# Kernel optimization log

Measured on AMD Instinct MI355X. Metric: run time of the kernel, lower is better.

## Reference

```python
import jax, jax.numpy as jnp
import numpy as np

N_NODES = 10000
N_EDGES = 200000
F = 128
NB = 20
LN_EPS = 1e-5

act = jax.nn.silu

def mlp2(x, W1, b1, W2, b2):
    # two-layer MLP: Linear -> silu -> Linear (weights stored [in, out])
    h = act(jnp.dot(x, W1) + b1)
    return jnp.dot(h, W2) + b2

def mlp2_nobias(x, W1, W2):
    return jnp.dot(act(jnp.dot(x, W1)), W2)

def layernorm(x, g, b):
    mu = jnp.mean(x, axis=-1, keepdims=True)
    var = jnp.mean(jnp.square(x - mu), axis=-1, keepdims=True)
    return (x - mu) * jax.lax.rsqrt(var + LN_EPS) * g + b

def setup_inputs() -> dict:
    key = jax.random.key(0)
    ks = jax.random.split(key, 32)
    s = 1.0 / np.sqrt(F)
    d = {
        "atom_node": jax.random.normal(ks[0], (N_NODES, F), jnp.float32),
        "force_node": jax.random.normal(ks[1], (N_NODES, 3, F), jnp.float32),
        "disp_node": jax.random.normal(ks[2], (N_NODES, 3, F), jnp.float32),
        "disp_edge": jax.random.normal(ks[3], (N_EDGES, 3), jnp.float32),
        "dist_edge": jax.random.uniform(ks[4], (N_EDGES, NB), jnp.float32),
        "edge_index": jax.random.randint(ks[5], (2, N_EDGES), 0, N_NODES, jnp.int32),
        # inv_message_nodepart
        "nmp_W1": jax.random.normal(ks[6], (F, F), jnp.float32) * s,
        "nmp_b1": jnp.zeros((F,), jnp.float32),
        "nmp_W2": jax.random.normal(ks[7], (F, F), jnp.float32) * s,
        "nmp_b2": jnp.zeros((F,), jnp.float32),
        # inv_message_edgepart
        "emp_W": jax.random.normal(ks[8], (NB, F), jnp.float32) * (1.0 / np.sqrt(NB)),
        "emp_b": jnp.zeros((F,), jnp.float32),
        # equiv_message1
        "eq1_W1": jax.random.normal(ks[9], (F, F), jnp.float32) * s,
        "eq1_b1": jnp.zeros((F,), jnp.float32),
        "eq1_W2": jax.random.normal(ks[10], (F, F), jnp.float32) * s,
        "eq1_b2": jnp.zeros((F,), jnp.float32),
        # equiv_message2
        "eq2_W1": jax.random.normal(ks[11], (F, F), jnp.float32) * s,
        "eq2_b1": jnp.zeros((F,), jnp.float32),
        "eq2_W2": jax.random.normal(ks[12], (F, F), jnp.float32) * s,
        "eq2_b2": jnp.zeros((F,), jnp.float32),
        # equiv_message3 (no bias)
        "eq3_W1": jax.random.normal(ks[13], (F, F), jnp.float32) * s,
        "eq3_W2": jax.random.normal(ks[14], (F, F), jnp.float32) * s,
        # inv_update
        "upd_W1": jax.random.normal(ks[15], (F, F), jnp.float32) * s,
        "upd_b1": jnp.zeros((F,), jnp.float32),
        "upd_W2": jax.random.normal(ks[16], (F, F), jnp.float32) * s,
        "upd_b2": jnp.zeros((F,), jnp.float32),
        # LayerNorm
        "ln_g": jnp.ones((F,), jnp.float32),
        "ln_b": jnp.zeros((F,), jnp.float32),
    }
    return d

def reference(atom_node, force_node, disp_node, disp_edge, dist_edge, edge_index,
              nmp_W1, nmp_b1, nmp_W2, nmp_b2, emp_W, emp_b,
              eq1_W1, eq1_b1, eq1_W2, eq1_b2,
              eq2_W1, eq2_b1, eq2_W2, eq2_b2,
              eq3_W1, eq3_W2,
              upd_W1, upd_b1, upd_W2, upd_b2,
              ln_g, ln_b):
    n = atom_node.shape[0]
    src = edge_index[0]
    dst = edge_index[1]
    seg = lambda x: jax.ops.segment_sum(x, src, num_segments=n)

    # invariant message: edge part * node parts gathered at both endpoints
    h = mlp2(atom_node, nmp_W1, nmp_b1, nmp_W2, nmp_b2)            # [N, F]
    e = jnp.dot(dist_edge, emp_W) + emp_b                           # [E, F]
    inv_message = e * h[src] * h[dst]                               # [E, F]
    atom_node = atom_node + seg(inv_message)

    # equivariant message 1: radial MLP * displacement vectors
    eq1 = mlp2(inv_message, eq1_W1, eq1_b1, eq1_W2, eq1_b2)[:, None, :] \
          * disp_edge[:, :, None]                                   # [E, 3, F]
    agg1 = seg(eq1)                                                 # [N, 3, F]
    force_node = force_node + agg1

    # equivariant message 2: edge MLP * neighbor displacement features (pre-update)
    eq2 = mlp2(inv_message, eq2_W1, eq2_b1, eq2_W2, eq2_b2)[:, None, :] \
          * disp_node[dst]                                          # [E, 3, F]
    disp_node = disp_node + seg(eq2)

    # equivariant message 3: scatter-then-gather of agg1 with invariant gate
    eq3_inv = mlp2_nobias(atom_node, eq3_W1, eq3_W2)                # [N, F]
    eq3 = eq3_inv[dst][:, None, :] * agg1[dst]                      # [E, 3, F]
    disp_node = disp_node + seg(eq3)

    # invariant update coupling force and displacement channels
    inv_update = mlp2(atom_node, upd_W1, upd_b1, upd_W2, upd_b2) \
                 * jnp.sum(-force_node * disp_node, axis=-2)        # [N, F]
    atom_node = layernorm(atom_node + inv_update, ln_g, ln_b)
    return (atom_node, force_node, disp_node)
```

## Files before the change

kernel.cpp:

```cpp
#include <hip/hip_runtime.h>
#include <hip/hip_bf16.h>

#define F 128
#define NB 20
#define KP 32
#define HSTRIDE 136
#define HROWS_STRIDE 140

typedef __attribute__((ext_vector_type(8))) short short8;
typedef __attribute__((ext_vector_type(4))) short short4v;
typedef __attribute__((ext_vector_type(4))) float floatx4;

__device__ __forceinline__ float silu_f(float x) {
    return x * __builtin_amdgcn_rcpf(1.0f + __expf(-x));
}
__device__ __forceinline__ float bfs2f(short s) {
    unsigned int u = ((unsigned int)(unsigned short)s) << 16;
    float f; __builtin_memcpy(&f, &u, 4); return f;
}
__device__ __forceinline__ float lo_bf(unsigned int u) { return bfs2f((short)(u & 0xFFFF)); }
__device__ __forceinline__ float hi_bf(unsigned int u) { return bfs2f((short)(u >> 16)); }
__device__ __forceinline__ unsigned int pack_bf2(float d, float v) {
    __hip_bfloat16 db = __float2bfloat16(d), vb = __float2bfloat16(v);
    return (unsigned int)*(unsigned short*)&db
         | ((unsigned int)*(unsigned short*)&vb << 16);
}

__device__ __forceinline__ void stage_issue(const __hip_bfloat16* W, int t,
                                            short8 wreg[4]) {
#pragma unroll
    for (int r = 0; r < 4; ++r)
        wreg[r] = *(const short8*)(W + (size_t)(r * 512 + t) * 8);
}
__device__ __forceinline__ void stage_write(__hip_bfloat16* wbuf, int t,
                                            const short8 wreg[4]) {
#pragma unroll
    for (int r = 0; r < 4; ++r) {
        const int c = r * 512 + t;
        *(short8*)(wbuf + (size_t)(c >> 4) * HSTRIDE + (c & 15) * 8) = wreg[r];
    }
}

template<typename OUT_T, bool BIAS>
__global__ __launch_bounds__(256) void fused_mlp_kernel(
    const __hip_bfloat16* __restrict__ X,
    const __hip_bfloat16* __restrict__ Wt1, const float* __restrict__ b1,
    const __hip_bfloat16* __restrict__ Wt2, const float* __restrict__ b2,
    OUT_T* __restrict__ Y, int Mp)
{
    __shared__ __hip_bfloat16 hid[128 * HSTRIDE];
    const int t = threadIdx.x;
    const int wave = t >> 6;
    const int lane = t & 63;
    const int quad = lane >> 4;
    const int l16  = lane & 15;
    const int eloc0 = wave * 32;
    const int e0 = blockIdx.x * 128 + eloc0;

    floatx4 acc[8][2];
#pragma unroll
    for (int ft = 0; ft < 8; ++ft)
#pragma unroll
        for (int et = 0; et < 2; ++et)
            acc[ft][et] = (floatx4){0.f, 0.f, 0.f, 0.f};

#pragma unroll
    for (int ks = 0; ks < 4; ++ks) {
        const int k0 = ks * 32 + quad * 8;
        short8 bx[2], aw[8];
#pragma unroll
        for (int et = 0; et < 2; ++et)
            bx[et] = *(const short8*)(X + (size_t)(e0 + et * 16 + l16) * F + k0);
#pragma unroll
        for (int ft = 0; ft < 8; ++ft)
            aw[ft] = *(const short8*)(Wt1 + (size_t)(ft * 16 + l16) * F + k0);
#pragma unroll
        for (int ft = 0; ft < 8; ++ft)
#pragma unroll
            for (int et = 0; et < 2; ++et)
                acc[ft][et] = __builtin_amdgcn_mfma_f32_16x16x32_bf16(
                    aw[ft], bx[et], acc[ft][et], 0, 0, 0);
    }

#pragma unroll
    for (int ft = 0; ft < 8; ++ft) {
        const int feat = ft * 16 + quad * 4;
        floatx4 bv = (floatx4){0.f, 0.f, 0.f, 0.f};
        if (BIAS) bv = *(const floatx4*)(b1 + feat);
#pragma unroll
        for (int et = 0; et < 2; ++et) {
            const int el = eloc0 + et * 16 + l16;
            __align__(8) __hip_bfloat16 tmp[4];
#pragma unroll
            for (int r = 0; r < 4; ++r)
                tmp[r] = __float2bfloat16(silu_f(acc[ft][et][r] + bv[r]));
            *(short4v*)(hid + (size_t)el * HSTRIDE + feat) = *(const short4v*)tmp;
        }
    }
    __builtin_amdgcn_sched_barrier(0);

#pragma unroll
    for (int ft = 0; ft < 8; ++ft)
#pragma unroll
        for (int et = 0; et < 2; ++et)
            acc[ft][et] = (floatx4){0.f, 0.f, 0.f, 0.f};

#pragma unroll
    for (int ks = 0; ks < 4; ++ks) {
        const int k0 = ks * 32 + quad * 8;
        short8 bx[2], aw[8];
#pragma unroll
        for (int et = 0; et < 2; ++et)
            bx[et] = *(const short8*)(hid + (size_t)(eloc0 + et * 16 + l16) * HSTRIDE + k0);
#pragma unroll
        for (int ft = 0; ft < 8; ++ft)
            aw[ft] = *(const short8*)(Wt2 + (size_t)(ft * 16 + l16) * F + k0);
#pragma unroll
        for (int ft = 0; ft < 8; ++ft)
#pragma unroll
            for (int et = 0; et < 2; ++et)
                acc[ft][et] = __builtin_amdgcn_mfma_f32_16x16x32_bf16(
                    aw[ft], bx[et], acc[ft][et], 0, 0, 0);
    }

#pragma unroll
    for (int ft = 0; ft < 8; ++ft) {
        const int feat = ft * 16 + quad * 4;
        floatx4 bv = (floatx4){0.f, 0.f, 0.f, 0.f};
        if (BIAS) bv = *(const floatx4*)(b2 + feat);
#pragma unroll
        for (int et = 0; et < 2; ++et) {
            const int e = e0 + et * 16 + l16;
            if (sizeof(OUT_T) == 2) {
                __align__(8) __hip_bfloat16 tmp[4];
#pragma unroll
                for (int r = 0; r < 4; ++r)
                    tmp[r] = __float2bfloat16(acc[ft][et][r] + bv[r]);
                *(short4v*)((__hip_bfloat16*)Y + (size_t)e * F + feat) = *(const short4v*)tmp;
            } else {
                floatx4 v;
#pragma unroll
                for (int r = 0; r < 4; ++r) v[r] = acc[ft][et][r] + bv[r];
                *(floatx4*)((float*)Y + (size_t)e * F + feat) = v;
            }
        }
    }
}

template<typename OUTA, typename OUTB, bool BIASA, bool BIASB>
__global__ __launch_bounds__(512, 4) void dual_mlp_kernel(
    const __hip_bfloat16* X,
    const __hip_bfloat16* __restrict__ W1a, const float* __restrict__ b1a,
    const __hip_bfloat16* __restrict__ W2a, const float* __restrict__ b2a,
    const __hip_bfloat16* __restrict__ W1b, const float* __restrict__ b1b,
    const __hip_bfloat16* __restrict__ W2b, const float* __restrict__ b2b,
    OUTA* __restrict__ Q1, OUTB* Q2, int Mp)
{
    __shared__ __hip_bfloat16 hid[128 * HSTRIDE];
    __shared__ __hip_bfloat16 wbuf[128 * HSTRIDE];
    const int t = threadIdx.x;
    const int wave = t >> 6;
    const int rg   = wave >> 1;
    const int wf   = wave & 1;
    const int lane = t & 63;
    const int quad = lane >> 4;
    const int l16  = lane & 15;
    const int eloc0 = rg * 32;
    const int e0 = blockIdx.x * 128 + eloc0;
    const int fbase = wf * 64;

    short8 bxk[4][2];
#pragma unroll
    for (int ks = 0; ks < 4; ++ks)
#pragma unroll
        for (int et = 0; et < 2; ++et)
            bxk[ks][et] = *(const short8*)(X + (size_t)(e0 + et * 16 + l16) * F
                                           + ks * 32 + quad * 8);

    short8 wreg[4];
    floatx4 acc[4][2];

    stage_issue(W1a, t, wreg);
    stage_write(wbuf, t, wreg);
    __syncthreads();

    stage_issue(W2a, t, wreg);
    __builtin_amdgcn_sched_barrier(0);
#pragma unroll
    for (int ft = 0; ft < 4; ++ft)
#pragma unroll
        for (int et = 0; et < 2; ++et)
            acc[ft][et] = (floatx4){0.f, 0.f, 0.f, 0.f};
#pragma unroll
    for (int ks = 0; ks < 4; ++ks) {
        const int k0 = ks * 32 + quad * 8;
        short8 aw[4];
#pragma unroll
        for (int ft = 0; ft < 4; ++ft)
            aw[ft] = *(const short8*)(wbuf + (size_t)(fbase + ft * 16 + l16) * HSTRIDE + k0);
#pragma unroll
        for (int ft = 0; ft < 4; ++ft)
#pragma unroll
            for (int et = 0; et < 2; ++et)
                acc[ft][et] = __builtin_amdgcn_mfma_f32_16x16x32_bf16(
                    aw[ft], bxk[ks][et], acc[ft][et], 0, 0, 0);
    }
#pragma unroll
    for (int ft = 0; ft < 4; ++ft) {
        const int feat = fbase + ft * 16 + quad * 4;
        floatx4 bv = (floatx4){0.f, 0.f, 0.f, 0.f};
        if (BIASA) bv = *(const floatx4*)(b1a + feat);
#pragma unroll
        for (int et = 0; et < 2; ++et) {
            const int el = eloc0 + et * 16 + l16;
            __align__(8) __hip_bfloat16 tmp[4];
#pragma unroll
            for (int r = 0; r < 4; ++r)
                tmp[r] = __float2bfloat16(silu_f(acc[ft][et][r] + bv[r]));
            *(short4v*)(hid + (size_t)el * HSTRIDE + feat) = *(const short4v*)tmp;
        }
    }
    __syncthreads();
    stage_write(wbuf, t, wreg);
    __syncthreads();

    stage_issue(W1b, t, wreg);
    __builtin_amdgcn_sched_barrier(0);
#pragma unroll
    for (int ft = 0; ft < 4; ++ft)
#pragma unroll
        for (int et = 0; et < 2; ++et)
            acc[ft][et] = (floatx4){0.f, 0.f, 0.f, 0.f};
#pragma unroll
    for (int ks = 0; ks < 4; ++ks) {
        const int k0 = ks * 32 + quad * 8;
        short8 bh[2], aw[4];
#pragma unroll
        for (int et = 0; et < 2; ++et)
            bh[et] = *(const short8*)(hid + (size_t)(eloc0 + et * 16 + l16) * HSTRIDE + k0);
#pragma unroll
        for (int ft = 0; ft < 4; ++ft)
            aw[ft] = *(const short8*)(wbuf + (size_t)(fbase + ft * 16 + l16) * HSTRIDE + k0);
#pragma unroll
        for (int ft = 0; ft < 4; ++ft)
#pragma unroll
            for (int et = 0; et < 2; ++et)
                acc[ft][et] = __builtin_amdgcn_mfma_f32_16x16x32_bf16(
                    aw[ft], bh[et], acc[ft][et], 0, 0, 0);
    }
#pragma unroll
    for (int ft = 0; ft < 4; ++ft) {
        const int feat = fbase + ft * 16 + quad * 4;
        floatx4 bv = (floatx4){0.f, 0.f, 0.f, 0.f};
        if (BIASA) bv = *(const floatx4*)(b2a + feat);
#pragma unroll
        for (int et = 0; et < 2; ++et) {
            const int e = e0 + et * 16 + l16;
            if (sizeof(OUTA) == 2) {
                __align__(8) __hip_bfloat16 tmp[4];
#pragma unroll
                for (int r = 0; r < 4; ++r)
                    tmp[r] = __float2bfloat16(acc[ft][et][r] + bv[r]);
                *(short4v*)((__hip_bfloat16*)Q1 + (size_t)e * F + feat) = *(const short4v*)tmp;
            } else {
                floatx4 v;
#pragma unroll
                for (int r = 0; r < 4; ++r) v[r] = acc[ft][et][r] + bv[r];
                *(floatx4*)((float*)Q1 + (size_t)e * F + feat) = v;
            }
        }
    }
    __syncthreads();
    stage_write(wbuf, t, wreg);
    __syncthreads();

    stage_issue(W2b, t, wreg);
    __builtin_amdgcn_sched_barrier(0);
#pragma unroll
    for (int ft = 0; ft < 4; ++ft)
#pragma unroll
        for (int et = 0; et < 2; ++et)
            acc[ft][et] = (floatx4){0.f, 0.f, 0.f, 0.f};
#pragma unroll
    for (int ks = 0; ks < 4; ++ks) {
        const int k0 = ks * 32 + quad * 8;
        short8 aw[4];
#pragma unroll
        for (int ft = 0; ft < 4; ++ft)
            aw[ft] = *(const short8*)(wbuf + (size_t)(fbase + ft * 16 + l16) * HSTRIDE + k0);
#pragma unroll
        for (int ft = 0; ft < 4; ++ft)
#pragma unroll
            for (int et = 0; et < 2; ++et)
                acc[ft][et] = __builtin_amdgcn_mfma_f32_16x16x32_bf16(
                    aw[ft], bxk[ks][et], acc[ft][et], 0, 0, 0);
    }
#pragma unroll
    for (int ft = 0; ft < 4; ++ft) {
        const int feat = fbase + ft * 16 + quad * 4;
        floatx4 bv = (floatx4){0.f, 0.f, 0.f, 0.f};
        if (BIASB) bv = *(const floatx4*)(b1b + feat);
#pragma unroll
        for (int et = 0; et < 2; ++et) {
            const int el = eloc0 + et * 16 + l16;
            __align__(8) __hip_bfloat16 tmp[4];
#pragma unroll
            for (int r = 0; r < 4; ++r)
                tmp[r] = __float2bfloat16(silu_f(acc[ft][et][r] + bv[r]));
            *(short4v*)(hid + (size_t)el * HSTRIDE + feat) = *(const short4v*)tmp;
        }
    }
    __syncthreads();
    stage_write(wbuf, t, wreg);
    __syncthreads();

#pragma unroll
    for (int ft = 0; ft < 4; ++ft)
#pragma unroll
        for (int et = 0; et < 2; ++et)
            acc[ft][et] = (floatx4){0.f, 0.f, 0.f, 0.f};
#pragma unroll
    for (int ks = 0; ks < 4; ++ks) {
        const int k0 = ks * 32 + quad * 8;
        short8 bh[2], aw[4];
#pragma unroll
        for (int et = 0; et < 2; ++et)
            bh[et] = *(const short8*)(hid + (size_t)(eloc0 + et * 16 + l16) * HSTRIDE + k0);
#pragma unroll
        for (int ft = 0; ft < 4; ++ft)
            aw[ft] = *(const short8*)(wbuf + (size_t)(fbase + ft * 16 + l16) * HSTRIDE + k0);
#pragma unroll
        for (int ft = 0; ft < 4; ++ft)
#pragma unroll
            for (int et = 0; et < 2; ++et)
                acc[ft][et] = __builtin_amdgcn_mfma_f32_16x16x32_bf16(
                    aw[ft], bh[et], acc[ft][et], 0, 0, 0);
    }
#pragma unroll
    for (int ft = 0; ft < 4; ++ft) {
        const int feat = fbase + ft * 16 + quad * 4;
        floatx4 bv = (floatx4){0.f, 0.f, 0.f, 0.f};
        if (BIASB) bv = *(const floatx4*)(b2b + feat);
#pragma unroll
        for (int et = 0; et < 2; ++et) {
            const int e = e0 + et * 16 + l16;
            if (sizeof(OUTB) == 2) {
                __align__(8) __hip_bfloat16 tmp[4];
#pragma unroll
                for (int r = 0; r < 4; ++r)
                    tmp[r] = __float2bfloat16(acc[ft][et][r] + bv[r]);
                *(short4v*)((__hip_bfloat16*)Q2 + (size_t)e * F + feat) = *(const short4v*)tmp;
            } else {
                floatx4 v;
#pragma unroll
                for (int r = 0; r < 4; ++r) v[r] = acc[ft][et][r] + bv[r];
                *(floatx4*)((float*)Q2 + (size_t)e * F + feat) = v;
            }
        }
    }
}

__global__ __launch_bounds__(256) void edge_inv_mfma_kernel(
    const __hip_bfloat16* __restrict__ dist_p,
    const __hip_bfloat16* __restrict__ empWt,
    const float* __restrict__ emp_b, const __hip_bfloat16* __restrict__ h,
    const int* __restrict__ src_p, const int* __restrict__ dst_p,
    __hip_bfloat16* __restrict__ Xbf, int E)
{
    __shared__ __hip_bfloat16 hrows[256 * HROWS_STRIDE];
    __shared__ int ridx[256];
    const int t = threadIdx.x;
    const int wave = t >> 6;
    const int lane = t & 63;
    const int quad = lane >> 4;
    const int l16  = lane & 15;
    const int e0b = blockIdx.x * 128;
    const int e0 = e0b + wave * 32;

    {
        const int le = (t < 128) ? t : (t - 128);
        const int e = e0b + le;
        const int idx = (e < E) ? ((t < 128) ? src_p[e] : dst_p[e]) : 0;
        ridx[t] = idx;
    }
    __syncthreads();

#pragma unroll
    for (int i = 0; i < 16; ++i) {
        const int idx = i * 256 + t;
        const int r = idx >> 4, part = idx & 15;
        const short8 v = *(const short8*)(h + (size_t)ridx[r] * F + part * 8);
        const short4v lo = __builtin_shufflevector(v, v, 0, 1, 2, 3);
        const short4v hi = __builtin_shufflevector(v, v, 4, 5, 6, 7);
        *(short4v*)(hrows + (size_t)r * HROWS_STRIDE + part * 8)     = lo;
        *(short4v*)(hrows + (size_t)r * HROWS_STRIDE + part * 8 + 4) = hi;
    }

    short8 bx[2], aw[8];
#pragma unroll
    for (int et = 0; et < 2; ++et)
        bx[et] = *(const short8*)(dist_p + (size_t)(e0 + et * 16 + l16) * KP + quad * 8);
#pragma unroll
    for (int ft = 0; ft < 8; ++ft)
        aw[ft] = *(const short8*)(empWt + (size_t)(ft * 16 + l16) * KP + quad * 8);

    floatx4 acc[8][2];
#pragma unroll
    for (int ft = 0; ft < 8; ++ft)
#pragma unroll
        for (int et = 0; et < 2; ++et)
            acc[ft][et] = __builtin_amdgcn_mfma_f32_16x16x32_bf16(
                aw[ft], bx[et], (floatx4){0.f, 0.f, 0.f, 0.f}, 0, 0, 0);

    __syncthreads();

    int eidx[2];
#pragma unroll
    for (int et = 0; et < 2; ++et) eidx[et] = e0 + et * 16 + l16;

#pragma unroll
    for (int ft = 0; ft < 8; ++ft) {
        const int feat = ft * 16 + quad * 4;
        const floatx4 bv = *(const floatx4*)(emp_b + feat);
#pragma unroll
        for (int et = 0; et < 2; ++et) {
            const int le = wave * 32 + et * 16 + l16;
            const short4v hs = *(const short4v*)(hrows + (size_t)le * HROWS_STRIDE + feat);
            const short4v hd = *(const short4v*)(hrows + (size_t)(128 + le) * HROWS_STRIDE + feat);
            const bool v = eidx[et] < E;
            __align__(8) __hip_bfloat16 tmp[4];
#pragma unroll
            for (int r = 0; r < 4; ++r) {
                const float m = v ? (acc[ft][et][r] + bv[r]) * bfs2f(hs[r]) * bfs2f(hd[r])
                                  : 0.0f;
                tmp[r] = __float2bfloat16(m);
            }
            *(short4v*)(Xbf + (size_t)eidx[et] * F + feat) = *(const short4v*)tmp;
        }
    }
}


__global__ void prep_weights_kernel(
    const float* __restrict__ W0, const float* __restrict__ W1,
    const float* __restrict__ W2, const float* __restrict__ W3,
    const float* __restrict__ W4, const float* __restrict__ W5,
    const float* __restrict__ W6, const float* __restrict__ W7,
    const float* __restrict__ W8, const float* __restrict__ W9,
    __hip_bfloat16* __restrict__ Wt)
{
    const int t = blockIdx.x * 256 + threadIdx.x;
    if (t >= 10 * F * F) return;
    const int w = t >> 14;
    const int idx = t & (F * F - 1);
    const int n = idx >> 7;
    const int k = idx & 127;
    const float* W = (w == 0) ? W0 : (w == 1) ? W1 : (w == 2) ? W2 : (w == 3) ? W3
                   : (w == 4) ? W4 : (w == 5) ? W5 : (w == 6) ? W6 : (w == 7) ? W7
                   : (w == 8) ? W8 : W9;
    Wt[t] = __float2bfloat16(W[k * F + n]);
}

__global__ void prep_empw_kernel(const float* __restrict__ emp_W,
                                 __hip_bfloat16* __restrict__ empWt)
{
    const int t = blockIdx.x * 256 + threadIdx.x;
    if (t >= F * KP) return;
    const int n = t >> 5;
    const int k = t & (KP - 1);
    empWt[t] = __float2bfloat16(k < NB ? emp_W[k * F + n] : 0.0f);
}

__global__ void cast_pad_kernel(const float* __restrict__ src,
                                __hip_bfloat16* __restrict__ dst,
                                int n_valid, int n_total)
{
    const int stride = gridDim.x * blockDim.x;
    for (int i = blockIdx.x * blockDim.x + threadIdx.x; i < n_total; i += stride)
        dst[i] = __float2bfloat16(i < n_valid ? src[i] : 0.0f);
}

__global__ void pad_zero_bf_kernel(__hip_bfloat16* __restrict__ dst,
                                   int from, int to)
{
    const int i = from + blockIdx.x * 256 + threadIdx.x;
    if (i < to) dst[i] = __float2bfloat16(0.0f);
}


__global__ void zero_counts_kernel(int* __restrict__ counts, int N) {
    const int stride = gridDim.x * blockDim.x;
    for (int i = blockIdx.x * blockDim.x + threadIdx.x; i < N; i += stride)
        counts[i] = 0;
}

__global__ void csr_count_kernel(const int* __restrict__ src,
                                 int* __restrict__ counts, int E) {
    const int stride = gridDim.x * blockDim.x;
    for (int e = blockIdx.x * blockDim.x + threadIdx.x; e < E; e += stride)
        atomicAdd(&counts[src[e]], 1);
}

__global__ __launch_bounds__(1024) void csr_scan_kernel(
    const int* __restrict__ counts, int* __restrict__ offsets,
    int* __restrict__ cursor, int N)
{
    constexpr int T = 1024;
    const int t = threadIdx.x;
    const int per = (N + T - 1) / T;
    const int base = t * per;
    int lsum = 0;
    for (int i = 0; i < per; ++i) {
        int idx = base + i;
        if (idx < N) lsum += counts[idx];
    }
    __shared__ int s[T];
    s[t] = lsum;
    __syncthreads();
    for (int off = 1; off < T; off <<= 1) {
        int v = (t >= off) ? s[t - off] : 0;
        __syncthreads();
        s[t] += v;
        __syncthreads();
    }
    int run = s[t] - lsum;
    for (int i = 0; i < per; ++i) {
        int idx = base + i;
        if (idx < N) {
            offsets[idx] = run;
            cursor[idx] = run;
            run += counts[idx];
        }
    }
    if (t == T - 1) offsets[N] = run;
}

__global__ void csr_perm_kernel(const int* __restrict__ src,
                                const int* __restrict__ dst,
                                const float* __restrict__ disp_edge,
                                const float* __restrict__ dist_edge,
                                int* __restrict__ cursor,
                                int* __restrict__ src_p,
                                int* __restrict__ dst_p,
                                float* __restrict__ de_p,
                                __hip_bfloat16* __restrict__ dist_p, int E) {
    const int stride = gridDim.x * blockDim.x;
    for (int e = blockIdx.x * blockDim.x + threadIdx.x; e < E; e += stride) {
        const int s = src[e];
        const int pos = atomicAdd(&cursor[s], 1);
        src_p[pos] = s;
        dst_p[pos] = dst[e];
        de_p[3 * pos + 0] = disp_edge[3 * e + 0];
        de_p[3 * pos + 1] = disp_edge[3 * e + 1];
        de_p[3 * pos + 2] = disp_edge[3 * e + 2];
        __align__(16) __hip_bfloat16 tmp[KP];
#pragma unroll
        for (int k = 0; k < KP; ++k)
            tmp[k] = __float2bfloat16(k < NB ? dist_edge[(size_t)e * NB + k] : 0.0f);
#pragma unroll
        for (int q = 0; q < 4; ++q)
            *(short8*)(dist_p + (size_t)pos * KP + q * 8) = ((const short8*)tmp)[q];
    }
}


__global__ __launch_bounds__(256) void gather_inv_kernel(
    const __hip_bfloat16* __restrict__ inv_msg, const int* __restrict__ offsets,
    const float* __restrict__ atom,
    float* __restrict__ atom_new, __hip_bfloat16* __restrict__ atom_new_bf, int N)
{
    const int n = blockIdx.x * 4 + (threadIdx.x >> 6);
    if (n >= N) return;
    const int f0 = (threadIdx.x & 63) * 2;
    const int p0 = offsets[n], p1 = offsets[n + 1];
    float a0 = 0.0f, a1 = 0.0f;
    for (int p = p0; p < p1; ++p) {
        const unsigned int u = *(const unsigned int*)(inv_msg + (size_t)p * F + f0);
        a0 += lo_bf(u);
        a1 += hi_bf(u);
    }
    const float2 av = *(const float2*)(atom + (size_t)n * F + f0);
    const float v0 = av.x + a0, v1 = av.y + a1;
    *(float2*)(atom_new + (size_t)n * F + f0) = make_float2(v0, v1);
    __hip_bfloat16 b0 = __float2bfloat16(v0), b1 = __float2bfloat16(v1);
    *(ushort2*)(atom_new_bf + (size_t)n * F + f0) =
        make_ushort2(*(unsigned short*)&b0, *(unsigned short*)&b1);
}

__global__ __launch_bounds__(256) void gather_eq1_kernel(
    const __hip_bfloat16* __restrict__ eqm, const float* __restrict__ de_p,
    const int* __restrict__ offsets,
    const float* __restrict__ force, const float* __restrict__ disp_node,
    const __hip_bfloat16* __restrict__ eq3i_bf,
    float* __restrict__ out_force, ushort2* __restrict__ pk, int N)
{
    const int n = blockIdx.x * 4 + (threadIdx.x >> 6);
    if (n >= N) return;
    const int f0 = (threadIdx.x & 63) * 2;
    const int p0 = offsets[n], p1 = offsets[n + 1];
    float a00 = 0.f, a01 = 0.f, a10 = 0.f, a11 = 0.f, a20 = 0.f, a21 = 0.f;
    for (int p = p0; p < p1; ++p) {
        const unsigned int u = *(const unsigned int*)(eqm + (size_t)p * F + f0);
        const float m0 = lo_bf(u), m1 = hi_bf(u);
        const float d0 = de_p[(size_t)p * 3 + 0];
        const float d1 = de_p[(size_t)p * 3 + 1];
        const float d2 = de_p[(size_t)p * 3 + 2];
        a00 = fmaf(m0, d0, a00); a01 = fmaf(m1, d0, a01);
        a10 = fmaf(m0, d1, a10); a11 = fmaf(m1, d1, a11);
        a20 = fmaf(m0, d2, a20); a21 = fmaf(m1, d2, a21);
    }
    const unsigned int ug = *(const unsigned int*)(eq3i_bf + (size_t)n * F + f0);
    const float g0 = lo_bf(ug), g1 = hi_bf(ug);
    const size_t b = (size_t)n * 3 * F + f0;

    float2 f;
    f = *(const float2*)(force + b);
    *(float2*)(out_force + b) = make_float2(f.x + a00, f.y + a01);
    f = *(const float2*)(force + b + F);
    *(float2*)(out_force + b + F) = make_float2(f.x + a10, f.y + a11);
    f = *(const float2*)(force + b + 2 * F);
    *(float2*)(out_force + b + 2 * F) = make_float2(f.x + a20, f.y + a21);

    float2 dn;
    dn = *(const float2*)(disp_node + b);
    *(uint2*)(pk + b) = make_uint2(pack_bf2(dn.x, g0 * a00), pack_bf2(dn.y, g1 * a01));
    dn = *(const float2*)(disp_node + b + F);
    *(uint2*)(pk + b + F) = make_uint2(pack_bf2(dn.x, g0 * a10), pack_bf2(dn.y, g1 * a11));
    dn = *(const float2*)(disp_node + b + 2 * F);
    *(uint2*)(pk + b + 2 * F) = make_uint2(pack_bf2(dn.x, g0 * a20), pack_bf2(dn.y, g1 * a21));
}

__global__ __launch_bounds__(256) void gather_eq23_kernel(
    const __hip_bfloat16* __restrict__ eqm2, const ushort2* __restrict__ pk,
    const float* __restrict__ disp_node,
    const int* __restrict__ dst_p, const int* __restrict__ offsets,
    float* __restrict__ out_disp, int N)
{
    const int n = blockIdx.x * 4 + (threadIdx.x >> 6);
    if (n >= N) return;
    const int f0 = (threadIdx.x & 63) * 2;
    const int p0 = offsets[n], p1 = offsets[n + 1];
    float a00 = 0.f, a01 = 0.f, a10 = 0.f, a11 = 0.f, a20 = 0.f, a21 = 0.f;
    int d = (p0 < p1) ? dst_p[p0] : 0;
    for (int p = p0; p < p1; ++p) {
        const int dn = (p + 1 < p1) ? dst_p[p + 1] : 0;
        const unsigned int u = *(const unsigned int*)(eqm2 + (size_t)p * F + f0);
        const float m0 = lo_bf(u), m1 = hi_bf(u);
        const size_t pb = (size_t)d * 3 * F + f0;
        const uint2 c0 = *(const uint2*)(pk + pb);
        const uint2 c1 = *(const uint2*)(pk + pb + F);
        const uint2 c2 = *(const uint2*)(pk + pb + 2 * F);
        a00 += m0 * lo_bf(c0.x) + hi_bf(c0.x);
        a01 += m1 * lo_bf(c0.y) + hi_bf(c0.y);
        a10 += m0 * lo_bf(c1.x) + hi_bf(c1.x);
        a11 += m1 * lo_bf(c1.y) + hi_bf(c1.y);
        a20 += m0 * lo_bf(c2.x) + hi_bf(c2.x);
        a21 += m1 * lo_bf(c2.y) + hi_bf(c2.y);
        d = dn;
    }
    const size_t b = (size_t)n * 3 * F + f0;
    float2 dn2;
    dn2 = *(const float2*)(disp_node + b);
    *(float2*)(out_disp + b) = make_float2(dn2.x + a00, dn2.y + a01);
    dn2 = *(const float2*)(disp_node + b + F);
    *(float2*)(out_disp + b + F) = make_float2(dn2.x + a10, dn2.y + a11);
    dn2 = *(const float2*)(disp_node + b + 2 * F);
    *(float2*)(out_disp + b + 2 * F) = make_float2(dn2.x + a20, dn2.y + a21);
}


__global__ __launch_bounds__(256) void update_ln_kernel(
    const float* __restrict__ atom_new, const float* __restrict__ upd,
    const float* __restrict__ out_force, const float* __restrict__ out_disp,
    const float* __restrict__ ln_g, const float* __restrict__ ln_b,
    float* __restrict__ out_atom, int N)
{
    const int n = blockIdx.x * 4 + (threadIdx.x >> 6);
    if (n >= N) return;
    const int f0 = (threadIdx.x & 63) * 2;
    const size_t b = (size_t)n * 3 * F + f0;

    const float2 fo0 = *(const float2*)(out_force + b);
    const float2 fo1 = *(const float2*)(out_force + b + F);
    const float2 fo2 = *(const float2*)(out_force + b + 2 * F);
    const float2 dl0 = *(const float2*)(out_disp + b);
    const float2 dl1 = *(const float2*)(out_disp + b + F);
    const float2 dl2 = *(const float2*)(out_disp + b + 2 * F);
    const float s0 = -(fo0.x * dl0.x + fo1.x * dl1.x + fo2.x * dl2.x);
    const float s1 = -(fo0.y * dl0.y + fo1.y * dl1.y + fo2.y * dl2.y);

    const float2 an = *(const float2*)(atom_new + (size_t)n * F + f0);
    const float2 up = *(const float2*)(upd + (size_t)n * F + f0);
    const float y0 = an.x + up.x * s0;
    const float y1 = an.y + up.y * s1;

    float sy = y0 + y1, syy = y0 * y0 + y1 * y1;
#pragma unroll
    for (int m = 1; m < 64; m <<= 1) {
        sy  += __shfl_xor(sy, m);
        syy += __shfl_xor(syy, m);
    }
    const float mu = sy * (1.0f / F);
    float var = syy * (1.0f / F) - mu * mu;
    if (var < 0.0f) var = 0.0f;
    const float rstd = rsqrtf(var + 1e-5f);

    const float2 gg = *(const float2*)(ln_g + f0);
    const float2 bb = *(const float2*)(ln_b + f0);
    *(float2*)(out_atom + (size_t)n * F + f0) =
        make_float2((y0 - mu) * rstd * gg.x + bb.x,
                    (y1 - mu) * rstd * gg.y + bb.y);
}

extern "C" void kernel_launch(void* const* d_in, const int* in_sizes, int n_in,
                              void* d_out, int out_size, void* d_ws, size_t ws_size,
                              hipStream_t stream)
{
    const float* atom_node  = (const float*)d_in[0];
    const float* force_node = (const float*)d_in[1];
    const float* disp_node  = (const float*)d_in[2];
    const float* disp_edge  = (const float*)d_in[3];
    const float* dist_edge  = (const float*)d_in[4];
    const int*   edge_index = (const int*)d_in[5];
    const float* nmp_W1 = (const float*)d_in[6];
    const float* nmp_b1 = (const float*)d_in[7];
    const float* nmp_W2 = (const float*)d_in[8];
    const float* nmp_b2 = (const float*)d_in[9];
    const float* emp_W  = (const float*)d_in[10];
    const float* emp_b  = (const float*)d_in[11];
    const float* eq1_W1 = (const float*)d_in[12];
    const float* eq1_b1 = (const float*)d_in[13];
    const float* eq1_W2 = (const float*)d_in[14];
    const float* eq1_b2 = (const float*)d_in[15];
    const float* eq2_W1 = (const float*)d_in[16];
    const float* eq2_b1 = (const float*)d_in[17];
    const float* eq2_W2 = (const float*)d_in[18];
    const float* eq2_b2 = (const float*)d_in[19];
    const float* eq3_W1 = (const float*)d_in[20];
    const float* eq3_W2 = (const float*)d_in[21];
    const float* upd_W1 = (const float*)d_in[22];
    const float* upd_b1 = (const float*)d_in[23];
    const float* upd_W2 = (const float*)d_in[24];
    const float* upd_b2 = (const float*)d_in[25];
    const float* ln_g   = (const float*)d_in[26];
    const float* ln_b   = (const float*)d_in[27];

    const int N = in_sizes[0] / F;
    const int E = in_sizes[4] / NB;
    const int Mp  = ((E + 127) / 128) * 128;
    const int Mp2 = ((N + 127) / 128) * 128;
    const int* src = edge_index;
    const int* dst = edge_index + E;
    const int nF = N * F, n3F = N * 3 * F;

    float* out_atom  = (float*)d_out;
    float* out_force = out_atom + (size_t)nF;
    float* out_disp  = out_force + (size_t)n3F;

    char* p = (char*)d_ws;
    int* counts  = (int*)p;
    int* offsets = counts + N;
    int* cursor  = offsets + (N + 1);
    int* src_p   = cursor + N;
    int* dst_p   = src_p + E;
    size_t off = (size_t)(3 * N + 1 + 2 * E) * sizeof(int);
    off = (off + 63) & ~(size_t)63;
    float* de_p = (float*)(p + off); off += (size_t)3 * E * sizeof(float);
    off = (off + 63) & ~(size_t)63;
    __hip_bfloat16* dist_p = (__hip_bfloat16*)(p + off); off += (size_t)Mp * KP * 2;
    __hip_bfloat16* empWt  = (__hip_bfloat16*)(p + off); off += (size_t)F * KP * 2;

    __hip_bfloat16* h_bf        = (__hip_bfloat16*)(p + off); off += (size_t)Mp2 * F * 2;
    __hip_bfloat16* atom_bf     = (__hip_bfloat16*)(p + off); off += (size_t)Mp2 * F * 2;
    __hip_bfloat16* atom_new_bf = (__hip_bfloat16*)(p + off); off += (size_t)Mp2 * F * 2;
    __hip_bfloat16* eq3i_bf     = (__hip_bfloat16*)(p + off); off += (size_t)Mp2 * F * 2;
    off = (off + 63) & ~(size_t)63;
    float* atom_new = (float*)(p + off); off += (size_t)nF * 4;
    float* upd_f    = (float*)(p + off); off += (size_t)Mp2 * F * 4;
    ushort2* pk     = (ushort2*)(p + off); off += (size_t)n3F * sizeof(ushort2);
    off = (off + 63) & ~(size_t)63;
    __hip_bfloat16* Xbf = (__hip_bfloat16*)(p + off); off += (size_t)Mp * F * 2;
    __hip_bfloat16* Q1  = (__hip_bfloat16*)(p + off); off += (size_t)Mp * F * 2;
    __hip_bfloat16* Q2  = Xbf;
    __hip_bfloat16* Wt  = (__hip_bfloat16*)(p + off);
    __hip_bfloat16* Wt_eq1a = Wt + 0 * F * F;
    __hip_bfloat16* Wt_eq1b = Wt + 1 * F * F;
    __hip_bfloat16* Wt_eq2a = Wt + 2 * F * F;
    __hip_bfloat16* Wt_eq2b = Wt + 3 * F * F;
    __hip_bfloat16* Wt_nmpa = Wt + 4 * F * F;
    __hip_bfloat16* Wt_nmpb = Wt + 5 * F * F;
    __hip_bfloat16* Wt_eq3a = Wt + 6 * F * F;
    __hip_bfloat16* Wt_eq3b = Wt + 7 * F * F;
    __hip_bfloat16* Wt_upda = Wt + 8 * F * F;
    __hip_bfloat16* Wt_updb = Wt + 9 * F * F;

    prep_weights_kernel<<<(10 * F * F + 255) / 256, 256, 0, stream>>>(
        eq1_W1, eq1_W2, eq2_W1, eq2_W2, nmp_W1, nmp_W2, eq3_W1, eq3_W2,
        upd_W1, upd_W2, Wt);
    prep_empw_kernel<<<(F * KP + 255) / 256, 256, 0, stream>>>(emp_W, empWt);
    cast_pad_kernel<<<512, 256, 0, stream>>>(atom_node, atom_bf, nF, Mp2 * F);
    pad_zero_bf_kernel<<<(Mp2 * F - nF + 255) / 256, 256, 0, stream>>>(
        atom_new_bf, nF, Mp2 * F);
    zero_counts_kernel<<<64, 256, 0, stream>>>(counts, N);
    csr_count_kernel<<<256, 256, 0, stream>>>(src, counts, E);
    csr_scan_kernel<<<1, 1024, 0, stream>>>(counts, offsets, cursor, N);
    csr_perm_kernel<<<256, 256, 0, stream>>>(src, dst, disp_edge, dist_edge,
                                             cursor, src_p, dst_p, de_p, dist_p, E);

    fused_mlp_kernel<__hip_bfloat16, true><<<Mp2 / 128, 256, 0, stream>>>(
        atom_bf, Wt_nmpa, nmp_b1, Wt_nmpb, nmp_b2, h_bf, Mp2);

    edge_inv_mfma_kernel<<<Mp / 128, 256, 0, stream>>>(
        dist_p, empWt, emp_b, h_bf, src_p, dst_p, Xbf, E);
    gather_inv_kernel<<<(N + 3) / 4, 256, 0, stream>>>(Xbf, offsets, atom_node,
                                                       atom_new, atom_new_bf, N);

    dual_mlp_kernel<__hip_bfloat16, float, false, true><<<Mp2 / 128, 512, 0, stream>>>(
        atom_new_bf, Wt_eq3a, nullptr, Wt_eq3b, nullptr,
        Wt_upda, upd_b1, Wt_updb, upd_b2, eq3i_bf, upd_f, Mp2);

    dual_mlp_kernel<__hip_bfloat16, __hip_bfloat16, true, true>
        <<<Mp / 128, 512, 0, stream>>>(
        Xbf, Wt_eq1a, eq1_b1, Wt_eq1b, eq1_b2,
        Wt_eq2a, eq2_b1, Wt_eq2b, eq2_b2, Q1, Q2, Mp);

    gather_eq1_kernel<<<(N + 3) / 4, 256, 0, stream>>>(
        Q1, de_p, offsets, force_node, disp_node, eq3i_bf, out_force, pk, N);
    gather_eq23_kernel<<<(N + 3) / 4, 256, 0, stream>>>(
        Q2, pk, disp_node, dst_p, offsets, out_disp, N);

    update_ln_kernel<<<(N + 3) / 4, 256, 0, stream>>>(
        atom_new, upd_f, out_force, out_disp, ln_g, ln_b, out_atom, N);
}
```

Measured before the change: 442.4 us.

## Merge node and edge dual-MLP launches, fragment-swizzle weight LDS, fuse LN into gather

Merges the two dual-MLP launches (node-side eq3/update and edge-side eq1/eq2) into one grid, choosing pointers at runtime by block index. Weight staging in LDS moves to a per-MFMA-fragment layout with an XOR swizzle, which removes the padded stride and is meant to cut LDS bank conflicts and shrink LDS use. The update+layernorm kernel is folded into the eq2/eq3 gather kernel, so out_disp is used from registers rather than reread. Runtime bias checks and selection branches add a little per-block overhead.

Result: faster. 424.7 us (-4.0%).

```diff
diff --git a/kernel.cpp b/kernel.cpp
--- a/kernel.cpp
+++ b/kernel.cpp
@@ -32,12 +32,16 @@
     for (int r = 0; r < 4; ++r)
         wreg[r] = *(const short8*)(W + (size_t)(r * 512 + t) * 8);
 }
-__device__ __forceinline__ void stage_write(__hip_bfloat16* wbuf, int t,
-                                            const short8 wreg[4]) {
+__device__ __forceinline__ void stage_write_frag(__hip_bfloat16* wbuf, int t,
+                                                 const short8 wreg[4]) {
 #pragma unroll
     for (int r = 0; r < 4; ++r) {
-        const int c = r * 512 + t;
-        *(short8*)(wbuf + (size_t)(c >> 4) * HSTRIDE + (c & 15) * 8) = wreg[r];
+        const int c0 = r * 512 + t;
+        const int n = c0 >> 4, p = c0 & 15;
+        const int ks = p >> 2;
+        const int frag = ((n >> 6) * 4 + ((n >> 4) & 3)) * 4 + ks;
+        const int lam = (((p & 3) * 16) + (n & 15)) ^ (ks << 1);
+        *(short8*)(wbuf + (size_t)frag * 512 + lam * 8) = wreg[r];
     }
 }
 
@@ -147,17 +151,34 @@
     }
 }
 
-template<typename OUTA, typename OUTB, bool BIASA, bool BIASB>
-__global__ __launch_bounds__(512, 4) void dual_mlp_kernel(
-    const __hip_bfloat16* X,
-    const __hip_bfloat16* __restrict__ W1a, const float* __restrict__ b1a,
-    const __hip_bfloat16* __restrict__ W2a, const float* __restrict__ b2a,
-    const __hip_bfloat16* __restrict__ W1b, const float* __restrict__ b1b,
-    const __hip_bfloat16* __restrict__ W2b, const float* __restrict__ b2b,
-    OUTA* __restrict__ Q1, OUTB* Q2, int Mp)
+__global__ __launch_bounds__(512, 4) void dual_mlp2_kernel(
+    const __hip_bfloat16* Xe,
+    const __hip_bfloat16* __restrict__ W1a_e, const float* __restrict__ b1a_e,
+    const __hip_bfloat16* __restrict__ W2a_e, const float* __restrict__ b2a_e,
+    const __hip_bfloat16* __restrict__ W1b_e, const float* __restrict__ b1b_e,
+    const __hip_bfloat16* __restrict__ W2b_e, const float* __restrict__ b2b_e,
+    __hip_bfloat16* __restrict__ Q1e, __hip_bfloat16* Q2e, int ntile_e,
+    const __hip_bfloat16* __restrict__ Xn,
+    const __hip_bfloat16* __restrict__ W1a_n,
+    const __hip_bfloat16* __restrict__ W2a_n,
+    const __hip_bfloat16* __restrict__ W1b_n, const float* __restrict__ b1b_n,
+    const __hip_bfloat16* __restrict__ W2b_n, const float* __restrict__ b2b_n,
+    __hip_bfloat16* __restrict__ Q1n, float* __restrict__ Q2n)
 {
     __shared__ __hip_bfloat16 hid[128 * HSTRIDE];
-    __shared__ __hip_bfloat16 wbuf[128 * HSTRIDE];
+    __shared__ __hip_bfloat16 wbuf[32 * 512];
+    const bool nn = (int)blockIdx.x >= ntile_e;
+    const int tile = nn ? ((int)blockIdx.x - ntile_e) : (int)blockIdx.x;
+    const __hip_bfloat16* X   = nn ? Xn : Xe;
+    const __hip_bfloat16* W1a = nn ? W1a_n : W1a_e;
+    const __hip_bfloat16* W2a = nn ? W2a_n : W2a_e;
+    const __hip_bfloat16* W1b = nn ? W1b_n : W1b_e;
+    const __hip_bfloat16* W2b = nn ? W2b_n : W2b_e;
+    const float* b1a = nn ? nullptr : b1a_e;
+    const float* b2a = nn ? nullptr : b2a_e;
+    const float* b1b = nn ? b1b_n : b1b_e;
+    const float* b2b = nn ? b2b_n : b2b_e;
+
     const int t = threadIdx.x;
     const int wave = t >> 6;
     const int rg   = wave >> 1;
@@ -166,7 +187,7 @@
     const int quad = lane >> 4;
     const int l16  = lane & 15;
     const int eloc0 = rg * 32;
-    const int e0 = blockIdx.x * 128 + eloc0;
+    const int e0 = tile * 128 + eloc0;
     const int fbase = wf * 64;
 
     short8 bxk[4][2];
@@ -181,7 +202,7 @@
     floatx4 acc[4][2];
 
     stage_issue(W1a, t, wreg);
-    stage_write(wbuf, t, wreg);
+    stage_write_frag(wbuf, t, wreg);
     __syncthreads();
 
     stage_issue(W2a, t, wreg);
@@ -193,11 +214,11 @@
             acc[ft][et] = (floatx4){0.f, 0.f, 0.f, 0.f};
 #pragma unroll
     for (int ks = 0; ks < 4; ++ks) {
-        const int k0 = ks * 32 + quad * 8;
         short8 aw[4];
 #pragma unroll
         for (int ft = 0; ft < 4; ++ft)
-            aw[ft] = *(const short8*)(wbuf + (size_t)(fbase + ft * 16 + l16) * HSTRIDE + k0);
+            aw[ft] = *(const short8*)(wbuf + ((wf * 4 + ft) * 4 + ks) * 512
+                                      + ((lane ^ (ks << 1)) * 8));
 #pragma unroll
         for (int ft = 0; ft < 4; ++ft)
 #pragma unroll
@@ -209,7 +230,7 @@
     for (int ft = 0; ft < 4; ++ft) {
         const int feat = fbase + ft * 16 + quad * 4;
         floatx4 bv = (floatx4){0.f, 0.f, 0.f, 0.f};
-        if (BIASA) bv = *(const floatx4*)(b1a + feat);
+        if (b1a) bv = *(const floatx4*)(b1a + feat);
 #pragma unroll
         for (int et = 0; et < 2; ++et) {
             const int el = eloc0 + et * 16 + l16;
@@ -221,7 +242,7 @@
         }
     }
     __syncthreads();
-    stage_write(wbuf, t, wreg);
+    stage_write_frag(wbuf, t, wreg);
     __syncthreads();
 
     stage_issue(W1b, t, wreg);
@@ -240,7 +261,8 @@
             bh[et] = *(const short8*)(hid + (size_t)(eloc0 + et * 16 + l16) * HSTRIDE + k0);
 #pragma unroll
         for (int ft = 0; ft < 4; ++ft)
-            aw[ft] = *(const short8*)(wbuf + (size_t)(fbase + ft * 16 + l16) * HSTRIDE + k0);
+            aw[ft] = *(const short8*)(wbuf + ((wf * 4 + ft) * 4 + ks) * 512
+                                      + ((lane ^ (ks << 1)) * 8));
 #pragma unroll
         for (int ft = 0; ft < 4; ++ft)
 #pragma unroll
@@ -252,26 +274,19 @@
     for (int ft = 0; ft < 4; ++ft) {
         const int feat = fbase + ft * 16 + quad * 4;
         floatx4 bv = (floatx4){0.f, 0.f, 0.f, 0.f};
-        if (BIASA) bv = *(const floatx4*)(b2a + feat);
+        if (b2a) bv = *(const floatx4*)(b2a + feat);
 #pragma unroll
         for (int et = 0; et < 2; ++et) {
             const int e = e0 + et * 16 + l16;
-            if (sizeof(OUTA) == 2) {
-                __align__(8) __hip_bfloat16 tmp[4];
-#pragma unroll
-                for (int r = 0; r < 4; ++r)
-                    tmp[r] = __float2bfloat16(acc[ft][et][r] + bv[r]);
-                *(short4v*)((__hip_bfloat16*)Q1 + (size_t)e * F + feat) = *(const short4v*)tmp;
-            } else {
-                floatx4 v;
-#pragma unroll
-                for (int r = 0; r < 4; ++r) v[r] = acc[ft][et][r] + bv[r];
-                *(floatx4*)((float*)Q1 + (size_t)e * F + feat) = v;
-            }
+            __align__(8) __hip_bfloat16 tmp[4];
+#pragma unroll
+            for (int r = 0; r < 4; ++r)
+                tmp[r] = __float2bfloat16(acc[ft][et][r] + bv[r]);
+            *(short4v*)((nn ? Q1n : Q1e) + (size_t)e * F + feat) = *(const short4v*)tmp;
         }
     }
     __syncthreads();
-    stage_write(wbuf, t, wreg);
+    stage_write_frag(wbuf, t, wreg);
     __syncthreads();
 
     stage_issue(W2b, t, wreg);
@@ -283,11 +298,11 @@
             acc[ft][et] = (floatx4){0.f, 0.f, 0.f, 0.f};
 #pragma unroll
     for (int ks = 0; ks < 4; ++ks) {
-        const int k0 = ks * 32 + quad * 8;
         short8 aw[4];
 #pragma unroll
         for (int ft = 0; ft < 4; ++ft)
-            aw[ft] = *(const short8*)(wbuf + (size_t)(fbase + ft * 16 + l16) * HSTRIDE + k0);
+            aw[ft] = *(const short8*)(wbuf + ((wf * 4 + ft) * 4 + ks) * 512
+                                      + ((lane ^ (ks << 1)) * 8));
 #pragma unroll
         for (int ft = 0; ft < 4; ++ft)
 #pragma unroll
@@ -299,7 +314,7 @@
     for (int ft = 0; ft < 4; ++ft) {
         const int feat = fbase + ft * 16 + quad * 4;
         floatx4 bv = (floatx4){0.f, 0.f, 0.f, 0.f};
-        if (BIASB) bv = *(const floatx4*)(b1b + feat);
+        if (b1b) bv = *(const floatx4*)(b1b + feat);
 #pragma unroll
         for (int et = 0; et < 2; ++et) {
             const int el = eloc0 + et * 16 + l16;
@@ -311,7 +326,7 @@
         }
     }
     __syncthreads();
-    stage_write(wbuf, t, wreg);
+    stage_write_frag(wbuf, t, wreg);
     __syncthreads();
 
 #pragma unroll
@@ -328,7 +343,8 @@
             bh[et] = *(const short8*)(hid + (size_t)(eloc0 + et * 16 + l16) * HSTRIDE + k0);
 #pragma unroll
         for (int ft = 0; ft < 4; ++ft)
-            aw[ft] = *(const short8*)(wbuf + (size_t)(fbase + ft * 16 + l16) * HSTRIDE + k0);
+            aw[ft] = *(const short8*)(wbuf + ((wf * 4 + ft) * 4 + ks) * 512
+                                      + ((lane ^ (ks << 1)) * 8));
 #pragma unroll
         for (int ft = 0; ft < 4; ++ft)
 #pragma unroll
@@ -340,21 +356,21 @@
     for (int ft = 0; ft < 4; ++ft) {
         const int feat = fbase + ft * 16 + quad * 4;
         floatx4 bv = (floatx4){0.f, 0.f, 0.f, 0.f};
-        if (BIASB) bv = *(const floatx4*)(b2b + feat);
+        if (b2b) bv = *(const floatx4*)(b2b + feat);
 #pragma unroll
         for (int et = 0; et < 2; ++et) {
             const int e = e0 + et * 16 + l16;
-            if (sizeof(OUTB) == 2) {
+            if (!nn) {
                 __align__(8) __hip_bfloat16 tmp[4];
 #pragma unroll
                 for (int r = 0; r < 4; ++r)
                     tmp[r] = __float2bfloat16(acc[ft][et][r] + bv[r]);
-                *(short4v*)((__hip_bfloat16*)Q2 + (size_t)e * F + feat) = *(const short4v*)tmp;
+                *(short4v*)(Q2e + (size_t)e * F + feat) = *(const short4v*)tmp;
             } else {
                 floatx4 v;
 #pragma unroll
                 for (int r = 0; r < 4; ++r) v[r] = acc[ft][et][r] + bv[r];
-                *(floatx4*)((float*)Q2 + (size_t)e * F + feat) = v;
+                *(floatx4*)(Q2n + (size_t)e * F + feat) = v;
             }
         }
     }
@@ -630,11 +646,14 @@
     *(uint2*)(pk + b + 2 * F) = make_uint2(pack_bf2(dn.x, g0 * a20), pack_bf2(dn.y, g1 * a21));
 }
 
-__global__ __launch_bounds__(256) void gather_eq23_kernel(
+__global__ __launch_bounds__(256) void gather_eq23_ln_kernel(
     const __hip_bfloat16* __restrict__ eqm2, const ushort2* __restrict__ pk,
     const float* __restrict__ disp_node,
     const int* __restrict__ dst_p, const int* __restrict__ offsets,
-    float* __restrict__ out_disp, int N)
+    const float* __restrict__ atom_new, const float* __restrict__ upd,
+    const float* __restrict__ out_force,
+    const float* __restrict__ ln_g, const float* __restrict__ ln_b,
+    float* __restrict__ out_disp, float* __restrict__ out_atom, int N)
 {
     const int n = blockIdx.x * 4 + (threadIdx.x >> 6);
     if (n >= N) return;
@@ -661,33 +680,20 @@
     const size_t b = (size_t)n * 3 * F + f0;
     float2 dn2;
     dn2 = *(const float2*)(disp_node + b);
-    *(float2*)(out_disp + b) = make_float2(dn2.x + a00, dn2.y + a01);
+    const float2 od0 = make_float2(dn2.x + a00, dn2.y + a01);
     dn2 = *(const float2*)(disp_node + b + F);
-    *(float2*)(out_disp + b + F) = make_float2(dn2.x + a10, dn2.y + a11);
+    const float2 od1 = make_float2(dn2.x + a10, dn2.y + a11);
     dn2 = *(const float2*)(disp_node + b + 2 * F);
-    *(float2*)(out_disp + b + 2 * F) = make_float2(dn2.x + a20, dn2.y + a21);
-}
-
-
-__global__ __launch_bounds__(256) void update_ln_kernel(
-    const float* __restrict__ atom_new, const float* __restrict__ upd,
-    const float* __restrict__ out_force, const float* __restrict__ out_disp,
-    const float* __restrict__ ln_g, const float* __restrict__ ln_b,
-    float* __restrict__ out_atom, int N)
-{
-    const int n = blockIdx.x * 4 + (threadIdx.x >> 6);
-    if (n >= N) return;
-    const int f0 = (threadIdx.x & 63) * 2;
-    const size_t b = (size_t)n * 3 * F + f0;
+    const float2 od2 = make_float2(dn2.x + a20, dn2.y + a21);
+    *(float2*)(out_disp + b)         = od0;
+    *(float2*)(out_disp + b + F)     = od1;
+    *(float2*)(out_disp + b + 2 * F) = od2;
 
     const float2 fo0 = *(const float2*)(out_force + b);
     const float2 fo1 = *(const float2*)(out_force + b + F);
     const float2 fo2 = *(const float2*)(out_force + b + 2 * F);
-    const float2 dl0 = *(const float2*)(out_disp + b);
-    const float2 dl1 = *(const float2*)(out_disp + b + F);
-    const float2 dl2 = *(const float2*)(out_disp + b + 2 * F);
-    const float s0 = -(fo0.x * dl0.x + fo1.x * dl1.x + fo2.x * dl2.x);
-    const float s1 = -(fo0.y * dl0.y + fo1.y * dl1.y + fo2.y * dl2.y);
+    const float s0 = -(fo0.x * od0.x + fo1.x * od1.x + fo2.x * od2.x);
+    const float s1 = -(fo0.y * od0.y + fo1.y * od1.y + fo2.y * od2.y);
 
     const float2 an = *(const float2*)(atom_new + (size_t)n * F + f0);
     const float2 up = *(const float2*)(upd + (size_t)n * F + f0);
@@ -815,20 +821,19 @@
     gather_inv_kernel<<<(N + 3) / 4, 256, 0, stream>>>(Xbf, offsets, atom_node,
                                                        atom_new, atom_new_bf, N);
 
-    dual_mlp_kernel<__hip_bfloat16, float, false, true><<<Mp2 / 128, 512, 0, stream>>>(
-        atom_new_bf, Wt_eq3a, nullptr, Wt_eq3b, nullptr,
-        Wt_upda, upd_b1, Wt_updb, upd_b2, eq3i_bf, upd_f, Mp2);
-
-    dual_mlp_kernel<__hip_bfloat16, __hip_bfloat16, true, true>
-        <<<Mp / 128, 512, 0, stream>>>(
-        Xbf, Wt_eq1a, eq1_b1, Wt_eq1b, eq1_b2,
-        Wt_eq2a, eq2_b1, Wt_eq2b, eq2_b2, Q1, Q2, Mp);
+    {
+        const int ntileE = Mp / 128;
+        const int ntileN = Mp2 / 128;
+        dual_mlp2_kernel<<<ntileE + ntileN, 512, 0, stream>>>(
+            Xbf, Wt_eq1a, eq1_b1, Wt_eq1b, eq1_b2,
+            Wt_eq2a, eq2_b1, Wt_eq2b, eq2_b2, Q1, Q2, ntileE,
+            atom_new_bf, Wt_eq3a, Wt_eq3b,
+            Wt_upda, upd_b1, Wt_updb, upd_b2, eq3i_bf, upd_f);
+    }
 
     gather_eq1_kernel<<<(N + 3) / 4, 256, 0, stream>>>(
         Q1, de_p, offsets, force_node, disp_node, eq3i_bf, out_force, pk, N);
-    gather_eq23_kernel<<<(N + 3) / 4, 256, 0, stream>>>(
-        Q2, pk, disp_node, dst_p, offsets, out_disp, N);
-
-    update_ln_kernel<<<(N + 3) / 4, 256, 0, stream>>>(
-        atom_new, upd_f, out_force, out_disp, ln_g, ln_b, out_atom, N);
-}
+    gather_eq23_ln_kernel<<<(N + 3) / 4, 256, 0, stream>>>(
+        Q2, pk, disp_node, dst_p, offsets, atom_new, upd_f, out_force,
+        ln_g, ln_b, out_disp, out_atom, N);
+}
```
